# Kernel tuning notes

Measured on AMD Instinct MI355X. Metric: run time of the kernel, lower is better.

Reference implementation:

```python
import jax, jax.numpy as jnp
import numpy as np

B, T, D, U = 32, 4096, 512, 512

def setup_inputs() -> dict:
    key = jax.random.key(0)
    ks = jax.random.split(key, 8)
    s = 0.02
    return {
        "query": jax.random.normal(ks[0], (B, D), dtype=jnp.float32),
        "values": jax.random.normal(ks[1], (B, T, D), dtype=jnp.float32),
        "W1": jax.random.normal(ks[2], (D, U), dtype=jnp.float32) * s,
        "b1": jnp.zeros((U,), dtype=jnp.float32),
        "W2": jax.random.normal(ks[3], (D, U), dtype=jnp.float32) * s,
        "b2": jnp.zeros((U,), dtype=jnp.float32),
        "V": jax.random.normal(ks[4], (U, 1), dtype=jnp.float32) * s,
        "bv": jnp.zeros((1,), dtype=jnp.float32),
    }

def reference(query, values, W1, b1, W2, b2, V, bv):
    # query: [B, D] -> [B, 1, U]; values: [B, T, D] -> [B, T, U]
    q_proj = (query @ W1 + b1)[:, None, :]            # [B, 1, U]
    v_proj = values @ W2 + b2                          # [B, T, U]
    scores = jnp.tanh(q_proj + v_proj) @ V + bv        # [B, T, 1]
    attn = jax.nn.softmax(scores, axis=1)              # softmax over time axis
    context = jnp.sum(attn * values, axis=1)           # [B, D]
    return context
```

## Files before the change

### kernel.cpp

```cpp
#include <hip/hip_runtime.h>
#include <hip/hip_bf16.h>
#include <math.h>

#define B_ 32
#define T_ 4096
#define D_ 512
#define U_ 512

typedef __bf16 bf16x8 __attribute__((ext_vector_type(8)));
typedef float floatx4 __attribute__((ext_vector_type(4)));
typedef unsigned short ushortx8 __attribute__((ext_vector_type(8)));

static __device__ __forceinline__ unsigned int f2bf(float f) {
  unsigned int u = __float_as_uint(f);
  return (u + 0x7fffu + ((u >> 16) & 1u)) >> 16;
}

static __device__ __forceinline__ float tanh_fast(float x) {
  float e = exp2f(x * 2.88539008178f);
  return 1.0f - 2.0f * __builtin_amdgcn_rcpf(1.0f + e);
}

static __device__ __forceinline__ uint4 pack8(const float4 a, const float4 b) {
  uint4 pk;
  pk.x = f2bf(a.x) | (f2bf(a.y) << 16);
  pk.y = f2bf(a.z) | (f2bf(a.w) << 16);
  pk.z = f2bf(b.x) | (f2bf(b.y) << 16);
  pk.w = f2bf(b.z) | (f2bf(b.w) << 16);
  return pk;
}

__global__ __launch_bounds__(256) void prep_w2b(
    const float* __restrict__ W2, unsigned short* __restrict__ W2B) {
  const int s = blockIdx.x * 256 + threadIdx.x;
  const int lane = s & 63;
  const int frag = s >> 6;
  const int ub = frag >> 4;
  const int kb = frag & 15;
  const int lr = lane & 15;
  const int kc = lane >> 4;
  const int u = ub * 16 + lr;
  const int k0 = kb * 32 + kc * 8;
  ushortx8 pk;
#pragma unroll
  for (int j = 0; j < 8; ++j)
    pk[j] = (unsigned short)f2bf(W2[(size_t)(k0 + j) * U_ + u]);
  *(ushortx8*)&W2B[(size_t)s * 8] = pk;
}

__global__ __launch_bounds__(256) void qproj_kernel(
    const float* __restrict__ query, const float* __restrict__ W1,
    const float* __restrict__ b1, const float* __restrict__ b2,
    float* __restrict__ qp) {
  const int b = blockIdx.x;
  const int tid = threadIdx.x;
  __shared__ float qs[D_];
  qs[tid] = query[b * D_ + tid];
  qs[tid + 256] = query[b * D_ + tid + 256];
  __syncthreads();
  const int u0 = tid * 2;
  float ax = 0.f, ay = 0.f;
#pragma unroll 8
  for (int k = 0; k < D_; ++k) {
    const float q = qs[k];
    const float2 w = *(const float2*)&W1[(size_t)k * U_ + u0];
    ax += q * w.x;
    ay += q * w.y;
  }
  qp[b * U_ + u0] = ax + b1[u0] + b2[u0];
  qp[b * U_ + u0 + 1] = ay + b1[u0 + 1] + b2[u0 + 1];
}

__global__ __launch_bounds__(256, 2) void scores_mfma(
    const float* __restrict__ values, const unsigned short* __restrict__ W2B,
    const float* __restrict__ qp, const float* __restrict__ V,
    float* __restrict__ scores) {
  const int b = blockIdx.y;
  const int t0 = blockIdx.x * 64;
  const int tid = threadIdx.x;
  const int w = tid >> 6;
  const int lane = tid & 63;
  const int lr = lane & 15;
  const int kc = lane >> 4;

  __shared__ __align__(16) unsigned short As[64 * 512];

  const float* vbase = values + ((size_t)b * T_ + t0) * D_;

#pragma unroll
  for (int p = 0; p < 16; ++p) {
    const int m = p * 256 + tid;
    const int r = m >> 6;
    const int k8 = m & 63;
    const float4 f0 = *(const float4*)&vbase[(size_t)r * D_ + k8 * 8];
    const float4 f1 = *(const float4*)&vbase[(size_t)r * D_ + k8 * 8 + 4];
    const int c = (k8 + r * 4) & 63;
    *(uint4*)&As[r * 512 + c * 8] = pack8(f0, f1);
  }
  __syncthreads();

  floatx4 acc[4][8];
#pragma unroll
  for (int i = 0; i < 4; ++i)
#pragma unroll
    for (int j = 0; j < 8; ++j) acc[i][j] = (floatx4)0.f;

  const ushortx8* W2Bv = (const ushortx8*)W2B;

#pragma unroll 4
  for (int ks = 0; ks < 16; ++ks) {
    bf16x8 bfr[8];
#pragma unroll
    for (int j = 0; j < 8; ++j)
      bfr[j] = __builtin_bit_cast(
          bf16x8, W2Bv[((w * 8 + j) * 16 + ks) * 64 + lane]);
    bf16x8 af[4];
#pragma unroll
    for (int i = 0; i < 4; ++i) {
      const int ri = i * 16 + lr;
      const int c = (ks * 4 + kc + ri * 4) & 63;
      af[i] = __builtin_bit_cast(bf16x8, *(ushortx8*)&As[ri * 512 + c * 8]);
    }
#pragma unroll
    for (int i = 0; i < 4; ++i)
#pragma unroll
      for (int j = 0; j < 8; ++j)
        acc[i][j] = __builtin_amdgcn_mfma_f32_16x16x32_bf16(af[i], bfr[j],
                                                            acc[i][j], 0, 0, 0);
  }

  const int no = w * 128;
  const float* qpb = qp + b * U_;
  float qv[8], vv[8];
#pragma unroll
  for (int j = 0; j < 8; ++j) {
    const int u = no + j * 16 + lr;
    qv[j] = qpb[u];
    vv[j] = V[u];
  }
  __syncthreads();
  float* red = (float*)As;
  const int mrow = (lane >> 4) * 4;
#pragma unroll
  for (int i = 0; i < 4; ++i) {
#pragma unroll
    for (int r = 0; r < 4; ++r) {
      float s = 0.f;
#pragma unroll
      for (int j = 0; j < 8; ++j) s += tanh_fast(acc[i][j][r] + qv[j]) * vv[j];
      s += __shfl_xor(s, 1);
      s += __shfl_xor(s, 2);
      s += __shfl_xor(s, 4);
      s += __shfl_xor(s, 8);
      if (lr == 0) red[w * 64 + i * 16 + mrow + r] = s;
    }
  }
  __syncthreads();
  if (tid < 64)
    scores[(size_t)b * T_ + t0 + tid] =
        red[tid] + red[64 + tid] + red[128 + tid] + red[192 + tid];
}

__global__ __launch_bounds__(256) void softmax_kernel(float* __restrict__ sc) {
  const int b = blockIdx.x;
  const int tid = threadIdx.x;
  __shared__ float red[256];
  float* s = sc + (size_t)b * T_;
  float v[16];
  float lmax = -1e30f;
#pragma unroll
  for (int i = 0; i < 16; ++i) {
    v[i] = s[tid + 256 * i];
    lmax = fmaxf(lmax, v[i]);
  }
  red[tid] = lmax;
  __syncthreads();
  for (int off = 128; off > 0; off >>= 1) {
    if (tid < off) red[tid] = fmaxf(red[tid], red[tid + off]);
    __syncthreads();
  }
  const float m = red[0];
  __syncthreads();
  float lsum = 0.f;
#pragma unroll
  for (int i = 0; i < 16; ++i) {
    v[i] = expf(v[i] - m);
    lsum += v[i];
  }
  red[tid] = lsum;
  __syncthreads();
  for (int off = 128; off > 0; off >>= 1) {
    if (tid < off) red[tid] += red[tid + off];
    __syncthreads();
  }
  const float inv = 1.0f / red[0];
#pragma unroll
  for (int i = 0; i < 16; ++i) s[tid + 256 * i] = v[i] * inv;
}

__global__ __launch_bounds__(256) void context_kernel(
    const float* __restrict__ values, const float* __restrict__ attn,
    float* __restrict__ out) {
  const int b = blockIdx.x;
  const int t0 = blockIdx.y * 128;
  const int tid = threadIdx.x;
  const int tx = tid & 127;
  const int ty = tid >> 7;
  __shared__ float as[128];
  __shared__ float4 red[128];
  if (tid < 128) as[tid] = attn[(size_t)b * T_ + t0 + tid];
  __syncthreads();
  const float* vb = values + ((size_t)b * T_ + t0) * D_;
  float ax = 0.f, ay = 0.f, az = 0.f, aw = 0.f;
#pragma unroll 8
  for (int t = ty; t < 128; t += 2) {
    const float a = as[t];
    const float4 v = *(const float4*)&vb[(size_t)t * D_ + tx * 4];
    ax += a * v.x;
    ay += a * v.y;
    az += a * v.z;
    aw += a * v.w;
  }
  if (ty == 1) red[tx] = make_float4(ax, ay, az, aw);
  __syncthreads();
  if (ty == 0) {
    const float4 o = red[tx];
    const int d = tx * 4;
    atomicAdd(&out[b * D_ + d],     ax + o.x);
    atomicAdd(&out[b * D_ + d + 1], ay + o.y);
    atomicAdd(&out[b * D_ + d + 2], az + o.z);
    atomicAdd(&out[b * D_ + d + 3], aw + o.w);
  }
}

extern "C" void kernel_launch(void* const* d_in, const int* in_sizes, int n_in,
                              void* d_out, int out_size, void* d_ws,
                              size_t ws_size, hipStream_t stream) {
  const float* query = (const float*)d_in[0];
  const float* values = (const float*)d_in[1];
  const float* W1 = (const float*)d_in[2];
  const float* b1 = (const float*)d_in[3];
  const float* W2 = (const float*)d_in[4];
  const float* b2 = (const float*)d_in[5];
  const float* V = (const float*)d_in[6];

  float* qp = (float*)d_ws;
  float* scores = qp + (size_t)B_ * U_;
  unsigned short* W2B = (unsigned short*)(scores + (size_t)B_ * T_);
  float* out = (float*)d_out;

  (void)hipMemsetAsync(d_out, 0, (size_t)B_ * D_ * sizeof(float), stream);

  prep_w2b<<<128, 256, 0, stream>>>(W2, W2B);
  qproj_kernel<<<B_, 256, 0, stream>>>(query, W1, b1, b2, qp);
  scores_mfma<<<dim3(T_ / 64, B_), 256, 0, stream>>>(values, W2B, qp, V,
                                                     scores);
  softmax_kernel<<<B_, 256, 0, stream>>>(scores);
  context_kernel<<<dim3(B_, 32), 256, 0, stream>>>(values, scores, out);
}
```

Before: 520.7 us.

## Double-buffer values tiles in scores kernel and fold softmax into context

The scores kernel becomes a persistent 512-thread block per 512 timesteps. It prefetches the next 64-row fp32 tile into registers while the MFMAs run on the current bf16 tile in LDS, using an XOR-swizzled layout. It writes exp(score) directly, so the separate softmax kernel is gone. The context kernel now reduces the exp sum itself before scaling. Query projection is split across the K dimension for more blocks. The risks: exp is taken without subtracting the max, which relies on the scores staying bounded; each CU now holds only one large-LDS block; and every context block recomputes the denominator.

Measured after the change: 527.5 us. No clear change (+1.3%).

```diff
diff --git a/kernel.cpp b/kernel.cpp
--- a/kernel.cpp
+++ b/kernel.cpp
@@ -53,153 +53,155 @@
     const float* __restrict__ b1, const float* __restrict__ b2,
     float* __restrict__ qp) {
   const int b = blockIdx.x;
+  const int ug = blockIdx.y;
   const int tid = threadIdx.x;
+  const int uq = tid & 63;
+  const int kq = tid >> 6;
   __shared__ float qs[D_];
+  __shared__ float red[4][64];
   qs[tid] = query[b * D_ + tid];
   qs[tid + 256] = query[b * D_ + tid + 256];
   __syncthreads();
-  const int u0 = tid * 2;
-  float ax = 0.f, ay = 0.f;
+  const int u = ug * 64 + uq;
+  float a = 0.f;
 #pragma unroll 8
-  for (int k = 0; k < D_; ++k) {
-    const float q = qs[k];
-    const float2 w = *(const float2*)&W1[(size_t)k * U_ + u0];
-    ax += q * w.x;
-    ay += q * w.y;
-  }
-  qp[b * U_ + u0] = ax + b1[u0] + b2[u0];
-  qp[b * U_ + u0 + 1] = ay + b1[u0 + 1] + b2[u0 + 1];
-}
-
-__global__ __launch_bounds__(256, 2) void scores_mfma(
+  for (int k = kq * 128; k < kq * 128 + 128; ++k)
+    a += qs[k] * W1[(size_t)k * U_ + u];
+  red[kq][uq] = a;
+  __syncthreads();
+  if (tid < 64) {
+    const int uu = ug * 64 + tid;
+    qp[b * U_ + uu] =
+        red[0][tid] + red[1][tid] + red[2][tid] + red[3][tid] + b1[uu] + b2[uu];
+  }
+}
+
+__global__ __launch_bounds__(512, 2) void scores_mfma(
     const float* __restrict__ values, const unsigned short* __restrict__ W2B,
     const float* __restrict__ qp, const float* __restrict__ V,
-    float* __restrict__ scores) {
+    float* __restrict__ wexp) {
+  __shared__ __align__(16) unsigned short As[2 * 64 * 512];
+  __shared__ float redp[2 * 512];
+
   const int b = blockIdx.y;
-  const int t0 = blockIdx.x * 64;
+  const int tg = blockIdx.x;
   const int tid = threadIdx.x;
   const int w = tid >> 6;
   const int lane = tid & 63;
   const int lr = lane & 15;
   const int kc = lane >> 4;
-
-  __shared__ __align__(16) unsigned short As[64 * 512];
-
-  const float* vbase = values + ((size_t)b * T_ + t0) * D_;
-
-#pragma unroll
-  for (int p = 0; p < 16; ++p) {
-    const int m = p * 256 + tid;
-    const int r = m >> 6;
-    const int k8 = m & 63;
-    const float4 f0 = *(const float4*)&vbase[(size_t)r * D_ + k8 * 8];
-    const float4 f1 = *(const float4*)&vbase[(size_t)r * D_ + k8 * 8 + 4];
-    const int c = (k8 + r * 4) & 63;
-    *(uint4*)&As[r * 512 + c * 8] = pack8(f0, f1);
-  }
-  __syncthreads();
-
-  floatx4 acc[4][8];
-#pragma unroll
-  for (int i = 0; i < 4; ++i)
-#pragma unroll
-    for (int j = 0; j < 8; ++j) acc[i][j] = (floatx4)0.f;
-
+  const int w4 = w * 4;
+
+  const float* vbase = values + ((size_t)b * T_ + (size_t)tg * 512) * D_;
   const ushortx8* W2Bv = (const ushortx8*)W2B;
 
-#pragma unroll 4
-  for (int ks = 0; ks < 16; ++ks) {
-    bf16x8 bfr[8];
-#pragma unroll
-    for (int j = 0; j < 8; ++j)
-      bfr[j] = __builtin_bit_cast(
-          bf16x8, W2Bv[((w * 8 + j) * 16 + ks) * 64 + lane]);
-    bf16x8 af[4];
-#pragma unroll
-    for (int i = 0; i < 4; ++i) {
-      const int ri = i * 16 + lr;
-      const int c = (ks * 4 + kc + ri * 4) & 63;
-      af[i] = __builtin_bit_cast(bf16x8, *(ushortx8*)&As[ri * 512 + c * 8]);
-    }
-#pragma unroll
-    for (int i = 0; i < 4; ++i)
-#pragma unroll
-      for (int j = 0; j < 8; ++j)
-        acc[i][j] = __builtin_amdgcn_mfma_f32_16x16x32_bf16(af[i], bfr[j],
-                                                            acc[i][j], 0, 0, 0);
-  }
-
-  const int no = w * 128;
+  float qv[4], vv[4];
   const float* qpb = qp + b * U_;
-  float qv[8], vv[8];
-#pragma unroll
-  for (int j = 0; j < 8; ++j) {
-    const int u = no + j * 16 + lr;
+#pragma unroll
+  for (int j = 0; j < 4; ++j) {
+    const int u = w * 64 + j * 16 + lr;
     qv[j] = qpb[u];
     vv[j] = V[u];
   }
-  __syncthreads();
-  float* red = (float*)As;
-  const int mrow = (lane >> 4) * 4;
-#pragma unroll
-  for (int i = 0; i < 4; ++i) {
-#pragma unroll
-    for (int r = 0; r < 4; ++r) {
-      float s = 0.f;
-#pragma unroll
-      for (int j = 0; j < 8; ++j) s += tanh_fast(acc[i][j][r] + qv[j]) * vv[j];
+
+  {
+#pragma unroll
+    for (int p = 0; p < 8; ++p) {
+      const int r = p * 8 + w;
+      const float* rp = vbase + (size_t)r * D_ + lane * 8;
+      const float4 f0 = *(const float4*)rp;
+      const float4 f1 = *(const float4*)(rp + 4);
+      *(uint4*)&As[r * 512 + (lane ^ w) * 8] = pack8(f0, f1);
+    }
+  }
+  __syncthreads();
+
+  for (int n = 0; n < 8; ++n) {
+    const int cur = n & 1;
+    const unsigned short* Asc = As + cur * 32768;
+
+    float4 sv[16];
+    if (n + 1 < 8) {
+      const float* tb = vbase + (size_t)(n + 1) * 64 * D_;
+#pragma unroll
+      for (int p = 0; p < 8; ++p) {
+        const float* rp = tb + (size_t)(p * 8 + w) * D_ + lane * 8;
+        sv[2 * p] = *(const float4*)rp;
+        sv[2 * p + 1] = *(const float4*)(rp + 4);
+      }
+    }
+
+    floatx4 acc[4][4];
+#pragma unroll
+    for (int i = 0; i < 4; ++i)
+#pragma unroll
+      for (int j = 0; j < 4; ++j) acc[i][j] = (floatx4)0.f;
+
+#pragma unroll 4
+    for (int ks = 0; ks < 16; ++ks) {
+      bf16x8 bfr[4];
+#pragma unroll
+      for (int j = 0; j < 4; ++j)
+        bfr[j] = __builtin_bit_cast(
+            bf16x8, W2Bv[((w4 + j) * 16 + ks) * 64 + lane]);
+      const int c = (ks * 4 + kc) ^ (lr & 7);
+      bf16x8 af[4];
+#pragma unroll
+      for (int i = 0; i < 4; ++i) {
+        const int ri = i * 16 + lr;
+        af[i] =
+            __builtin_bit_cast(bf16x8, *(const ushortx8*)&Asc[ri * 512 + c * 8]);
+      }
+#pragma unroll
+      for (int i = 0; i < 4; ++i)
+#pragma unroll
+        for (int j = 0; j < 4; ++j)
+          acc[i][j] = __builtin_amdgcn_mfma_f32_16x16x32_bf16(
+              af[i], bfr[j], acc[i][j], 0, 0, 0);
+    }
+
+#pragma unroll
+    for (int i = 0; i < 4; ++i) {
+#pragma unroll
+      for (int r = 0; r < 4; ++r) {
+        float s = 0.f;
+#pragma unroll
+        for (int j = 0; j < 4; ++j) s += tanh_fast(acc[i][j][r] + qv[j]) * vv[j];
+        s += __shfl_xor(s, 1);
+        s += __shfl_xor(s, 2);
+        s += __shfl_xor(s, 4);
+        s += __shfl_xor(s, 8);
+        if (lr == 0) redp[cur * 512 + w * 64 + i * 16 + kc * 4 + r] = s;
+      }
+    }
+
+    if (n + 1 < 8) {
+      unsigned short* Asn = As + (cur ^ 1) * 32768;
+      const int c = lane ^ w;
+#pragma unroll
+      for (int p = 0; p < 8; ++p) {
+        const int r = p * 8 + w;
+        *(uint4*)&Asn[r * 512 + c * 8] = pack8(sv[2 * p], sv[2 * p + 1]);
+      }
+    }
+
+    __syncthreads();
+
+    {
+      const int row = tid >> 3;
+      const int p = tid & 7;
+      float s = redp[cur * 512 + p * 64 + row];
       s += __shfl_xor(s, 1);
       s += __shfl_xor(s, 2);
       s += __shfl_xor(s, 4);
-      s += __shfl_xor(s, 8);
-      if (lr == 0) red[w * 64 + i * 16 + mrow + r] = s;
-    }
-  }
-  __syncthreads();
-  if (tid < 64)
-    scores[(size_t)b * T_ + t0 + tid] =
-        red[tid] + red[64 + tid] + red[128 + tid] + red[192 + tid];
-}
-
-__global__ __launch_bounds__(256) void softmax_kernel(float* __restrict__ sc) {
-  const int b = blockIdx.x;
-  const int tid = threadIdx.x;
-  __shared__ float red[256];
-  float* s = sc + (size_t)b * T_;
-  float v[16];
-  float lmax = -1e30f;
-#pragma unroll
-  for (int i = 0; i < 16; ++i) {
-    v[i] = s[tid + 256 * i];
-    lmax = fmaxf(lmax, v[i]);
-  }
-  red[tid] = lmax;
-  __syncthreads();
-  for (int off = 128; off > 0; off >>= 1) {
-    if (tid < off) red[tid] = fmaxf(red[tid], red[tid + off]);
-    __syncthreads();
-  }
-  const float m = red[0];
-  __syncthreads();
-  float lsum = 0.f;
-#pragma unroll
-  for (int i = 0; i < 16; ++i) {
-    v[i] = expf(v[i] - m);
-    lsum += v[i];
-  }
-  red[tid] = lsum;
-  __syncthreads();
-  for (int off = 128; off > 0; off >>= 1) {
-    if (tid < off) red[tid] += red[tid + off];
-    __syncthreads();
-  }
-  const float inv = 1.0f / red[0];
-#pragma unroll
-  for (int i = 0; i < 16; ++i) s[tid + 256 * i] = v[i] * inv;
+      if (p == 0)
+        wexp[(size_t)b * T_ + tg * 512 + n * 64 + row] = expf(s);
+    }
+  }
 }
 
 __global__ __launch_bounds__(256) void context_kernel(
-    const float* __restrict__ values, const float* __restrict__ attn,
+    const float* __restrict__ values, const float* __restrict__ wexp,
     float* __restrict__ out) {
   const int b = blockIdx.x;
   const int t0 = blockIdx.y * 128;
@@ -207,9 +209,21 @@
   const int tx = tid & 127;
   const int ty = tid >> 7;
   __shared__ float as[128];
-  __shared__ float4 red[128];
-  if (tid < 128) as[tid] = attn[(size_t)b * T_ + t0 + tid];
-  __syncthreads();
+  __shared__ float4 redv[128];
+  __shared__ float dred[4];
+
+  const float* wb = wexp + (size_t)b * T_;
+  float lsum = 0.f;
+#pragma unroll
+  for (int i = 0; i < 16; ++i) lsum += wb[i * 256 + tid];
+#pragma unroll
+  for (int off = 1; off < 64; off <<= 1) lsum += __shfl_xor(lsum, off);
+  if ((tid & 63) == 0) dred[tid >> 6] = lsum;
+  __syncthreads();
+  const float scale = 1.0f / (dred[0] + dred[1] + dred[2] + dred[3]);
+  if (tid < 128) as[tid] = wb[t0 + tid] * scale;
+  __syncthreads();
+
   const float* vb = values + ((size_t)b * T_ + t0) * D_;
   float ax = 0.f, ay = 0.f, az = 0.f, aw = 0.f;
 #pragma unroll 8
@@ -221,10 +235,10 @@
     az += a * v.z;
     aw += a * v.w;
   }
-  if (ty == 1) red[tx] = make_float4(ax, ay, az, aw);
+  if (ty == 1) redv[tx] = make_float4(ax, ay, az, aw);
   __syncthreads();
   if (ty == 0) {
-    const float4 o = red[tx];
+    const float4 o = redv[tx];
     const int d = tx * 4;
     atomicAdd(&out[b * D_ + d],     ax + o.x);
     atomicAdd(&out[b * D_ + d + 1], ay + o.y);
@@ -245,16 +259,14 @@
   const float* V = (const float*)d_in[6];
 
   float* qp = (float*)d_ws;
-  float* scores = qp + (size_t)B_ * U_;
-  unsigned short* W2B = (unsigned short*)(scores + (size_t)B_ * T_);
+  float* wexp = qp + (size_t)B_ * U_;
+  unsigned short* W2B = (unsigned short*)(wexp + (size_t)B_ * T_);
   float* out = (float*)d_out;
 
   (void)hipMemsetAsync(d_out, 0, (size_t)B_ * D_ * sizeof(float), stream);
 
   prep_w2b<<<128, 256, 0, stream>>>(W2, W2B);
-  qproj_kernel<<<B_, 256, 0, stream>>>(query, W1, b1, b2, qp);
-  scores_mfma<<<dim3(T_ / 64, B_), 256, 0, stream>>>(values, W2B, qp, V,
-                                                     scores);
-  softmax_kernel<<<B_, 256, 0, stream>>>(scores);
-  context_kernel<<<dim3(B_, 32), 256, 0, stream>>>(values, scores, out);
-}
+  qproj_kernel<<<dim3(B_, 8), 256, 0, stream>>>(query, W1, b1, b2, qp);
+  scores_mfma<<<dim3(8, B_), 512, 0, stream>>>(values, W2B, qp, V, wexp);
+  context_kernel<<<dim3(B_, 32), 256, 0, stream>>>(values, wexp, out);
+}
```
